# Optimization experiments

Hardware: AMD Instinct MI355X
Metric: run time of the kernel (lower is better)

The kernel has to match this reference:

```python
import jax, jax.numpy as jnp
import numpy as np

D_IN = 1024
D_OUT = 1024


def setup_inputs() -> dict:
    key = jax.random.key(0)
    kx, kq, kk, kv = jax.random.split(key, 4)
    x = jax.random.normal(kx, (4, 2048, D_IN), dtype=jnp.float32)
    s = 1.0 / np.sqrt(D_IN)
    Wq = jax.random.normal(kq, (D_IN, D_OUT), dtype=jnp.float32) * s
    Wk = jax.random.normal(kk, (D_IN, D_OUT), dtype=jnp.float32) * s
    Wv = jax.random.normal(kv, (D_IN, D_OUT), dtype=jnp.float32) * s
    return {"x": x, "Wq": Wq, "Wk": Wk, "Wv": Wv}


def reference(x, Wq, Wk, Wv):
    # x: [B, S, d_in]; W*: [d_in, d_out]
    B, S, _ = x.shape
    q = x @ Wq  # [B, S, d_out]
    k = x @ Wk
    v = x @ Wv
    scale = 1.0 / jnp.sqrt(jnp.asarray(k.shape[-1], x.dtype))
    scores = jnp.einsum("bqd,bkd->bqk", q, k) * scale  # [B, S, S]
    # causal mask: positions j > i masked to -inf (triu, diagonal=1)
    causal = jnp.tril(jnp.ones((S, S), dtype=bool))
    scores = jnp.where(causal[None, :, :], scores, -jnp.inf)
    attn = jax.nn.softmax(scores, axis=-1)  # dropout p=0.0 -> identity
    return jnp.einsum("bqk,bkd->bqd", attn, v)
```

## Files before the change

### kernel.cpp

```cpp
#include <hip/hip_runtime.h>
#include <hip/hip_bf16.h>

#define NB 4
#define SB 2048
#define DD 1024
#define BM 128
#define BN 128
#define BK 32

typedef __attribute__((ext_vector_type(8))) short bf16x8;
typedef __attribute__((ext_vector_type(4))) short bf16x4;
typedef __attribute__((ext_vector_type(4))) float f32x4;
typedef unsigned int u32;

__device__ __forceinline__ float bf2f(unsigned short u) {
    return __uint_as_float(((u32)u) << 16);
}
__device__ __forceinline__ short f2bf(float f) {
    u32 u = __float_as_uint(f);
    u32 r = (u + 0x7fffu + ((u >> 16) & 1u)) >> 16;
    return (short)r;
}

__device__ __forceinline__ void mfma_step(const short* As, const short* Bs,
                                          f32x4 (&acc)[4][4], int lane, int wave)
{
    const int wm = (wave >> 1) * 64, wn = (wave & 1) * 64;
    const int fr = lane & 15;
    const int quad = lane >> 4;
    bf16x8 af[4], bf[4];
#pragma unroll
    for (int t = 0; t < 4; t++) {
        af[t] = *(const bf16x8*)&As[(wm + t * 16 + fr) * BK + quad * 8];
        bf[t] = *(const bf16x8*)&Bs[(wn + t * 16 + fr) * BK + quad * 8];
    }
#pragma unroll
    for (int mt = 0; mt < 4; mt++)
#pragma unroll
        for (int nt = 0; nt < 4; nt++)
            acc[mt][nt] = __builtin_amdgcn_mfma_f32_16x16x32_bf16(
                af[mt], bf[nt], acc[mt][nt], 0, 0, 0);
}

__device__ __forceinline__ void mfma_step_pv(const short* As, const short* Bs,
                                             f32x4 (&acc)[2][4], int lane,
                                             int wave)
{
    const int wm = wave * 32;
    const int fr = lane & 15;
    const int quad = lane >> 4;
    bf16x8 af[2], bf[4];
#pragma unroll
    for (int t = 0; t < 2; t++)
        af[t] = *(const bf16x8*)&As[(wm + t * 16 + fr) * BK + quad * 8];
#pragma unroll
    for (int t = 0; t < 4; t++)
        bf[t] = *(const bf16x8*)&Bs[(t * 16 + fr) * BK + quad * 8];
#pragma unroll
    for (int mt = 0; mt < 2; mt++)
#pragma unroll
        for (int nt = 0; nt < 4; nt++)
            acc[mt][nt] = __builtin_amdgcn_mfma_f32_16x16x32_bf16(
                af[mt], bf[nt], acc[mt][nt], 0, 0, 0);
}

__device__ __forceinline__ void stage128x32(const short* __restrict__ g, int ld,
                                            short* lds, int tid) {
    const int wave = tid >> 6, lane = tid & 63;
    const int r = lane >> 2;
    const int c = (lane & 3) * 8;
#pragma unroll
    for (int i = 0; i < 2; i++) {
        const int chunk = wave * 2 + i;
        const short* gp = g + (size_t)(chunk * 16 + r) * ld + c;
        __builtin_amdgcn_global_load_lds(
            (const __attribute__((address_space(1))) u32*)gp,
            (__attribute__((address_space(3))) u32*)(lds + chunk * 512 + lane * 8),
            16, 0, 0);
    }
}

__device__ __forceinline__ void stage64x32(const short* __restrict__ g, int ld,
                                           short* lds, int tid) {
    const int wave = tid >> 6, lane = tid & 63;
    const int r = lane >> 2;
    const int c = (lane & 3) * 8;
    const short* gp = g + (size_t)(wave * 16 + r) * ld + c;
    __builtin_amdgcn_global_load_lds(
        (const __attribute__((address_space(1))) u32*)gp,
        (__attribute__((address_space(3))) u32*)(lds + wave * 512 + lane * 8),
        16, 0, 0);
}

__device__ __forceinline__ void stage_f32_128x32(const float* __restrict__ g,
                                                 int ld, short* lds, int tid) {
    const int r = tid >> 1;
    const int c = (tid & 1) * 16;
    const float* gp = &g[(size_t)r * ld + c];
    float4 v0 = *(const float4*)(gp + 0);
    float4 v1 = *(const float4*)(gp + 4);
    float4 v2 = *(const float4*)(gp + 8);
    float4 v3 = *(const float4*)(gp + 12);
    bf16x8 o0, o1;
    o0[0] = f2bf(v0.x); o0[1] = f2bf(v0.y); o0[2] = f2bf(v0.z); o0[3] = f2bf(v0.w);
    o0[4] = f2bf(v1.x); o0[5] = f2bf(v1.y); o0[6] = f2bf(v1.z); o0[7] = f2bf(v1.w);
    o1[0] = f2bf(v2.x); o1[1] = f2bf(v2.y); o1[2] = f2bf(v2.z); o1[3] = f2bf(v2.w);
    o1[4] = f2bf(v3.x); o1[5] = f2bf(v3.y); o1[6] = f2bf(v3.z); o1[7] = f2bf(v3.w);
    *(bf16x8*)&lds[r * BK + c] = o0;
    *(bf16x8*)&lds[r * BK + c + 8] = o1;
}

__device__ __forceinline__ void gemm_bt_body2(
    const short* __restrict__ A, int lda, const short* __restrict__ Bt, int ldb,
    int m0, int n0, int kend, short* As, short* Bs, f32x4 (&acc)[4][4], int tid)
{
    const int lane = tid & 63;
    const int wave = tid >> 6;
    const short* Ap = A + (size_t)m0 * lda;
    const short* Bp = Bt + (size_t)n0 * ldb;
    for (int k0 = 0; k0 < kend; k0 += 2 * BK) {
        stage128x32(Ap + k0, lda, As, tid);
        stage128x32(Ap + k0 + BK, lda, As + BM * BK, tid);
        stage128x32(Bp + k0, ldb, Bs, tid);
        stage128x32(Bp + k0 + BK, ldb, Bs + BN * BK, tid);
        __syncthreads();
        mfma_step(As, Bs, acc, lane, wave);
        mfma_step(As + BM * BK, Bs + BN * BK, acc, lane, wave);
        __syncthreads();
    }
}

__global__ __launch_bounds__(256) void prep_mm(
    const float* __restrict__ x, const float* __restrict__ Wq,
    const float* __restrict__ Wk, const float* __restrict__ Wv,
    short* __restrict__ xb, short* __restrict__ Wvt, float* __restrict__ Mp4)
{
    __shared__ short As[BM * BK], Bs[BN * BK];
    __shared__ short t[64][65];
    const int bx = blockIdx.x;
    const int tid = threadIdx.x;
    if (bx < 256) {
        const int ch = bx >> 6;
        const int t64 = bx & 63;
        const int m0 = (t64 >> 3) * BM;
        const int n0 = (t64 & 7) * BN;
        const int kbase = ch * 256;
        const int lane = tid & 63, wave = tid >> 6;
        f32x4 acc[4][4];
#pragma unroll
        for (int a = 0; a < 4; a++)
#pragma unroll
            for (int b = 0; b < 4; b++) acc[a][b] = (f32x4){0.f, 0.f, 0.f, 0.f};
        for (int k0 = 0; k0 < 256; k0 += BK) {
            stage_f32_128x32(Wk + (size_t)m0 * DD + kbase + k0, DD, As, tid);
            stage_f32_128x32(Wq + (size_t)n0 * DD + kbase + k0, DD, Bs, tid);
            __syncthreads();
            mfma_step(As, Bs, acc, lane, wave);
            __syncthreads();
        }
        const int wm = (wave >> 1) * 64, wn = (wave & 1) * 64;
        const int fr = lane & 15, quad = lane >> 4;
        float* Mc = Mp4 + (size_t)ch * DD * DD;
#pragma unroll
        for (int mt = 0; mt < 4; mt++)
#pragma unroll
            for (int nt = 0; nt < 4; nt++)
#pragma unroll
                for (int r = 0; r < 4; r++) {
                    const size_t m = m0 + wm + mt * 16 + quad * 4 + r;
                    const size_t n = n0 + wn + nt * 16 + fr;
                    Mc[m * DD + n] = acc[mt][nt][r];
                }
        return;
    }
    if (bx < 4352) {
        const size_t i = ((size_t)(bx - 256) * 256 + tid) * 8;
        float4 a = *(const float4*)&x[i];
        float4 b = *(const float4*)&x[i + 4];
        bf16x8 o;
        o[0] = f2bf(a.x); o[1] = f2bf(a.y); o[2] = f2bf(a.z); o[3] = f2bf(a.w);
        o[4] = f2bf(b.x); o[5] = f2bf(b.y); o[6] = f2bf(b.z); o[7] = f2bf(b.w);
        *(bf16x8*)&xb[i] = o;
        return;
    }
    const int rr = bx - 4352;
    const int k0 = (rr & 15) * 64;
    const int n0 = (rr >> 4) * 64;
    {
        const int r = tid >> 4;
        const int c = (tid & 15) * 4;
#pragma unroll
        for (int i = 0; i < 4; i++) {
            float4 v = *(const float4*)&Wv[(size_t)(k0 + i * 16 + r) * DD + n0 + c];
            t[i * 16 + r][c + 0] = f2bf(v.x);
            t[i * 16 + r][c + 1] = f2bf(v.y);
            t[i * 16 + r][c + 2] = f2bf(v.z);
            t[i * 16 + r][c + 3] = f2bf(v.w);
        }
    }
    __syncthreads();
    {
        const int r = tid >> 3;
        const int c = (tid & 7) * 8;
#pragma unroll
        for (int i = 0; i < 2; i++) {
            bf16x8 o;
#pragma unroll
            for (int j = 0; j < 8; j++) o[j] = t[c + j][i * 32 + r];
            *(bf16x8*)&Wvt[(size_t)(n0 + i * 32 + r) * DD + k0 + c] = o;
        }
    }
}

__global__ __launch_bounds__(256) void mm_reduce(const float* __restrict__ Mp4,
                                                 short* __restrict__ Mp)
{
    const size_t e = ((size_t)blockIdx.x * 256 + threadIdx.x) * 4;
    const size_t N = (size_t)DD * DD;
    float4 s = *(const float4*)&Mp4[e];
#pragma unroll
    for (int c = 1; c < 4; c++) {
        float4 p = *(const float4*)&Mp4[c * N + e];
        s.x += p.x; s.y += p.y; s.z += p.z; s.w += p.w;
    }
    bf16x4 o;
    o[0] = f2bf(s.x); o[1] = f2bf(s.y); o[2] = f2bf(s.z); o[3] = f2bf(s.w);
    *(bf16x4*)&Mp[e] = o;
}

__global__ __launch_bounds__(256) void tv_gemm(
    const short* __restrict__ xb, const short* __restrict__ Mp,
    const short* __restrict__ Wvt, short* __restrict__ T,
    short* __restrict__ Vt)
{
    __shared__ short As[2 * BM * BK], Bs[2 * BN * BK];
    const int lin = blockIdx.x + 8 * blockIdx.y;
    const int swz = (lin & 7) * 64 + (lin >> 3);
    const int n0 = (swz & 7) * BN;
    const int m0 = (swz >> 3) * BM;
    const int isv = blockIdx.z;
    const short* Bt = isv ? Wvt : Mp;
    f32x4 acc[4][4];
#pragma unroll
    for (int a = 0; a < 4; a++)
#pragma unroll
        for (int b = 0; b < 4; b++) acc[a][b] = (f32x4){0.f, 0.f, 0.f, 0.f};
    gemm_bt_body2(xb, DD, Bt, DD, m0, n0, DD, As, Bs, acc, threadIdx.x);
    const int lane = threadIdx.x & 63, wave = threadIdx.x >> 6;
    const int wm = (wave >> 1) * 64, wn = (wave & 1) * 64;
    const int fr = lane & 15, quad = lane >> 4;
    if (!isv) {
#pragma unroll
        for (int mt = 0; mt < 4; mt++)
#pragma unroll
            for (int nt = 0; nt < 4; nt++)
#pragma unroll
                for (int r = 0; r < 4; r++) {
                    const size_t m = m0 + wm + mt * 16 + quad * 4 + r;
                    const size_t n = n0 + wn + nt * 16 + fr;
                    T[m * DD + n] = f2bf(acc[mt][nt][r]);
                }
    } else {
        const int bb = m0 >> 11;
        const int s0 = (m0 & (SB - 1)) + wm + quad * 4;
        short* Vb = Vt + (size_t)bb * DD * SB;
#pragma unroll
        for (int mt = 0; mt < 4; mt++)
#pragma unroll
            for (int nt = 0; nt < 4; nt++) {
                const size_t n = n0 + wn + nt * 16 + fr;
                const size_t s = s0 + mt * 16;
                bf16x4 o;
#pragma unroll
                for (int r = 0; r < 4; r++) o[r] = f2bf(acc[mt][nt][r]);
                *(bf16x4*)&Vb[n * SB + s] = o;
            }
    }
}

__global__ __launch_bounds__(256) void scores_mfma(
    const short* __restrict__ T, const short* __restrict__ xb,
    short* __restrict__ Sc)
{
    const int bx = blockIdx.x;
    const int idx = (bx & 7) * 17 + (bx >> 3);
    int qt = (int)((__fsqrt_rn(8.f * idx + 1.f) - 1.f) * 0.5f);
    while ((qt + 1) * (qt + 2) / 2 <= idx) qt++;
    while (qt * (qt + 1) / 2 > idx) qt--;
    const int kt = idx - qt * (qt + 1) / 2;
    const int qm0 = qt * BM;
    const int kn0 = kt * BN;
    const int b = blockIdx.y;
    __shared__ short As[2 * BM * BK], Bs[2 * BN * BK];
    const short* Tb = T + (size_t)b * SB * DD;
    const short* Xb = xb + (size_t)b * SB * DD;
    short* Sb = Sc + (size_t)b * SB * SB;
    f32x4 acc[4][4];
#pragma unroll
    for (int a = 0; a < 4; a++)
#pragma unroll
        for (int c = 0; c < 4; c++) acc[a][c] = (f32x4){0.f, 0.f, 0.f, 0.f};
    gemm_bt_body2(Tb, DD, Xb, DD, qm0, kn0, DD, As, Bs, acc, threadIdx.x);
    const int lane = threadIdx.x & 63, wave = threadIdx.x >> 6;
    const int wm = (wave >> 1) * 64, wn = (wave & 1) * 64;
    const int fr = lane & 15, quad = lane >> 4;
    const float scale = 0.03125f;
#pragma unroll
    for (int mt = 0; mt < 4; mt++)
#pragma unroll
        for (int nt = 0; nt < 4; nt++)
#pragma unroll
            for (int r = 0; r < 4; r++) {
                const size_t q = qm0 + wm + mt * 16 + quad * 4 + r;
                const size_t k = kn0 + wn + nt * 16 + fr;
                Sb[q * SB + k] = f2bf(acc[mt][nt][r] * scale);
            }
}

__global__ __launch_bounds__(256) void softmax_kernel(short* __restrict__ Sc)
{
    const int row = blockIdx.x;
    const int i = row & (SB - 1);
    const int jlim = ((i >> 7) + 1) << 7;
    short* r = Sc + (size_t)row * SB;
    const int t = threadIdx.x;
    const int lane = t & 63, wave = t >> 6;
    __shared__ float red[8];

    const int j0 = t * 8;
    bf16x8 in = {0, 0, 0, 0, 0, 0, 0, 0};
    if (j0 <= i) in = *(const bf16x8*)&r[j0];
    float v[8];
    float mx = -1e30f;
#pragma unroll
    for (int e = 0; e < 8; e++) {
        const float s = (j0 + e <= i) ? bf2f((unsigned short)in[e]) : -1e30f;
        v[e] = s;
        mx = fmaxf(mx, s);
    }
#pragma unroll
    for (int o = 32; o > 0; o >>= 1) mx = fmaxf(mx, __shfl_down(mx, o));
    if (lane == 0) red[wave] = mx;
    __syncthreads();
    mx = fmaxf(fmaxf(red[0], red[1]), fmaxf(red[2], red[3]));

    float sum = 0.f;
#pragma unroll
    for (int e = 0; e < 8; e++) {
        const float x = (j0 + e <= i) ? __expf(v[e] - mx) : 0.f;
        v[e] = x;
        sum += x;
    }
#pragma unroll
    for (int o = 32; o > 0; o >>= 1) sum += __shfl_down(sum, o);
    if (lane == 0) red[4 + wave] = sum;
    __syncthreads();
    const float inv = 1.0f / (red[4] + red[5] + red[6] + red[7]);
    if (j0 < jlim) {
        bf16x8 o;
#pragma unroll
        for (int e = 0; e < 8; e++) o[e] = f2bf(v[e] * inv);
        *(bf16x8*)&r[j0] = o;
    }
}

__global__ __launch_bounds__(256) void pv_mfma(
    const short* __restrict__ P, const short* __restrict__ Vt,
    float* __restrict__ O)
{
    __shared__ short As[2 * BM * BK], Bs[2 * 64 * BK];
    const int n0 = blockIdx.x * 64;
    const int pair = blockIdx.y;
    const int b = blockIdx.z;
    const short* Pb = P + (size_t)b * SB * SB;
    const short* Vb = Vt + (size_t)b * DD * SB;
    float* Ob = O + (size_t)b * SB * DD;
    const int tid = threadIdx.x;
    const int lane = tid & 63, wave = tid >> 6;
    const int fr = lane & 15, quad = lane >> 4;
    for (int half = 0; half < 2; ++half) {
        const int qt = half ? (15 - pair) : pair;
        const int qm0 = qt * BM;
        const int kend = (qt + 1) * BM;
        const short* Pq = Pb + (size_t)qm0 * SB;
        const short* Vn = Vb + (size_t)n0 * SB;
        f32x4 acc[2][4];
#pragma unroll
        for (int a = 0; a < 2; a++)
#pragma unroll
            for (int c = 0; c < 4; c++) acc[a][c] = (f32x4){0.f, 0.f, 0.f, 0.f};
        for (int k0 = 0; k0 < kend; k0 += 2 * BK) {
            stage128x32(Pq + k0, SB, As, tid);
            stage128x32(Pq + k0 + BK, SB, As + BM * BK, tid);
            stage64x32(Vn + k0, SB, Bs, tid);
            stage64x32(Vn + k0 + BK, SB, Bs + 64 * BK, tid);
            __syncthreads();
            mfma_step_pv(As, Bs, acc, lane, wave);
            mfma_step_pv(As + BM * BK, Bs + 64 * BK, acc, lane, wave);
            __syncthreads();
        }
#pragma unroll
        for (int mt = 0; mt < 2; mt++)
#pragma unroll
            for (int nt = 0; nt < 4; nt++)
#pragma unroll
                for (int r = 0; r < 4; r++) {
                    const size_t q = qm0 + wave * 32 + mt * 16 + quad * 4 + r;
                    const size_t n = n0 + nt * 16 + fr;
                    Ob[q * DD + n] = acc[mt][nt][r];
                }
    }
}

extern "C" void kernel_launch(void* const* d_in, const int* in_sizes, int n_in,
                              void* d_out, int out_size, void* d_ws, size_t ws_size,
                              hipStream_t stream)
{
    const float* x  = (const float*)d_in[0];
    const float* Wq = (const float*)d_in[1];
    const float* Wk = (const float*)d_in[2];
    const float* Wv = (const float*)d_in[3];
    float* out = (float*)d_out;

    const size_t XE = (size_t)NB * SB * DD;
    const size_t WE = (size_t)DD * DD;
    short* xb  = (short*)d_ws;
    short* T   = xb + XE;
    short* Vt  = T + XE;
    short* Sc  = Vt + XE;
    float* Pp  = (float*)(Sc + (size_t)NB * SB * SB);
    short* Wvt = (short*)(Pp + (size_t)NB * 1024 * DD);
    short* Mp  = Wvt + WE;
    float* Mp4 = (float*)Sc;

    prep_mm<<<dim3(256 + 4096 + 256), 256, 0, stream>>>(
        x, Wq, Wk, Wv, xb, Wvt, Mp4);
    mm_reduce<<<dim3(1024), 256, 0, stream>>>(Mp4, Mp);
    tv_gemm<<<dim3(DD / BN, (NB * SB) / BM, 2), 256, 0, stream>>>(
        xb, Mp, Wvt, T, Vt);
    scores_mfma<<<dim3(136, NB), 256, 0, stream>>>(T, xb, Sc);
    softmax_kernel<<<dim3(NB * SB), 256, 0, stream>>>(Sc);
    pv_mfma<<<dim3(DD / 64, 8, NB), 256, 0, stream>>>(Sc, Vt, out);
}
```

Measured before the change: 231.2 us.

## Double-buffer LDS staging with manual vmcnt waits in GEMM and PV loops

Replaces the load-all-then-compute loops, which handled two K-slices per iteration, with a software-pipelined double-buffered loop. It prefetches the next BK slice into the alternate LDS buffer while MFMAs run on the current one. Explicit s_waitcnt vmcnt counts and raw s_barrier calls replace __syncthreads, so only the older loads must finish before the barrier. The aim is to hide global-load latency behind matrix math. The risk is that the hand-set vmcnt values assume a fixed number of outstanding loads per stage, and any extra compiler-emitted memory operation would break that.

```diff
diff --git a/kernel.cpp b/kernel.cpp
--- a/kernel.cpp
+++ b/kernel.cpp
@@ -20,6 +20,20 @@
     u32 u = __float_as_uint(f);
     u32 r = (u + 0x7fffu + ((u >> 16) & 1u)) >> 16;
     return (short)r;
+}
+
+__device__ __forceinline__ void wait_vm4() {
+    asm volatile("s_waitcnt vmcnt(4)" ::: "memory");
+}
+__device__ __forceinline__ void wait_vm3() {
+    asm volatile("s_waitcnt vmcnt(3)" ::: "memory");
+}
+__device__ __forceinline__ void wait_vm0() {
+    asm volatile("s_waitcnt vmcnt(0)" ::: "memory");
+}
+__device__ __forceinline__ void barrier_raw() {
+    __builtin_amdgcn_s_barrier();
+    asm volatile("" ::: "memory");
 }
 
 __device__ __forceinline__ void mfma_step(const short* As, const short* Bs,
@@ -110,23 +124,28 @@
     *(bf16x8*)&lds[r * BK + c + 8] = o1;
 }
 
-__device__ __forceinline__ void gemm_bt_body2(
+__device__ __forceinline__ void gemm_bt_cnt(
     const short* __restrict__ A, int lda, const short* __restrict__ Bt, int ldb,
-    int m0, int n0, int kend, short* As, short* Bs, f32x4 (&acc)[4][4], int tid)
+    int kend, short* As, short* Bs, f32x4 (&acc)[4][4], int tid)
 {
     const int lane = tid & 63;
     const int wave = tid >> 6;
-    const short* Ap = A + (size_t)m0 * lda;
-    const short* Bp = Bt + (size_t)n0 * ldb;
-    for (int k0 = 0; k0 < kend; k0 += 2 * BK) {
-        stage128x32(Ap + k0, lda, As, tid);
-        stage128x32(Ap + k0 + BK, lda, As + BM * BK, tid);
-        stage128x32(Bp + k0, ldb, Bs, tid);
-        stage128x32(Bp + k0 + BK, ldb, Bs + BN * BK, tid);
-        __syncthreads();
-        mfma_step(As, Bs, acc, lane, wave);
-        mfma_step(As + BM * BK, Bs + BN * BK, acc, lane, wave);
-        __syncthreads();
+    stage128x32(A, lda, As, tid);
+    stage128x32(Bt, ldb, Bs, tid);
+    for (int k0 = 0; k0 < kend; k0 += BK) {
+        const int cur = (k0 >> 5) & 1;
+        const short* as = As + cur * (BM * BK);
+        const short* bs = Bs + cur * (BN * BK);
+        if (k0 + BK < kend) {
+            stage128x32(A + k0 + BK, lda, As + (cur ^ 1) * (BM * BK), tid);
+            stage128x32(Bt + k0 + BK, ldb, Bs + (cur ^ 1) * (BN * BK), tid);
+            wait_vm4();
+        } else {
+            wait_vm0();
+        }
+        barrier_raw();
+        mfma_step(as, bs, acc, lane, wave);
+        barrier_raw();
     }
 }
 
@@ -245,7 +264,8 @@
     for (int a = 0; a < 4; a++)
 #pragma unroll
         for (int b = 0; b < 4; b++) acc[a][b] = (f32x4){0.f, 0.f, 0.f, 0.f};
-    gemm_bt_body2(xb, DD, Bt, DD, m0, n0, DD, As, Bs, acc, threadIdx.x);
+    gemm_bt_cnt(xb + (size_t)m0 * DD, DD, Bt + (size_t)n0 * DD, DD, DD,
+                As, Bs, acc, threadIdx.x);
     const int lane = threadIdx.x & 63, wave = threadIdx.x >> 6;
     const int wm = (wave >> 1) * 64, wn = (wave & 1) * 64;
     const int fr = lane & 15, quad = lane >> 4;
@@ -300,7 +320,8 @@
     for (int a = 0; a < 4; a++)
 #pragma unroll
         for (int c = 0; c < 4; c++) acc[a][c] = (f32x4){0.f, 0.f, 0.f, 0.f};
-    gemm_bt_body2(Tb, DD, Xb, DD, qm0, kn0, DD, As, Bs, acc, threadIdx.x);
+    gemm_bt_cnt(Tb + (size_t)qm0 * DD, DD, Xb + (size_t)kn0 * DD, DD, DD,
+                As, Bs, acc, threadIdx.x);
     const int lane = threadIdx.x & 63, wave = threadIdx.x >> 6;
     const int wm = (wave >> 1) * 64, wn = (wave & 1) * 64;
     const int fr = lane & 15, quad = lane >> 4;
@@ -389,15 +410,22 @@
         for (int a = 0; a < 2; a++)
 #pragma unroll
             for (int c = 0; c < 4; c++) acc[a][c] = (f32x4){0.f, 0.f, 0.f, 0.f};
-        for (int k0 = 0; k0 < kend; k0 += 2 * BK) {
-            stage128x32(Pq + k0, SB, As, tid);
-            stage128x32(Pq + k0 + BK, SB, As + BM * BK, tid);
-            stage64x32(Vn + k0, SB, Bs, tid);
-            stage64x32(Vn + k0 + BK, SB, Bs + 64 * BK, tid);
-            __syncthreads();
-            mfma_step_pv(As, Bs, acc, lane, wave);
-            mfma_step_pv(As + BM * BK, Bs + 64 * BK, acc, lane, wave);
-            __syncthreads();
+        stage128x32(Pq, SB, As, tid);
+        stage64x32(Vn, SB, Bs, tid);
+        for (int k0 = 0; k0 < kend; k0 += BK) {
+            const int cur = (k0 >> 5) & 1;
+            const short* as = As + cur * (BM * BK);
+            const short* bs = Bs + cur * (64 * BK);
+            if (k0 + BK < kend) {
+                stage128x32(Pq + k0 + BK, SB, As + (cur ^ 1) * (BM * BK), tid);
+                stage64x32(Vn + k0 + BK, SB, Bs + (cur ^ 1) * (64 * BK), tid);
+                wait_vm3();
+            } else {
+                wait_vm0();
+            }
+            barrier_raw();
+            mfma_step_pv(as, bs, acc, lane, wave);
+            barrier_raw();
         }
 #pragma unroll
         for (int mt = 0; mt < 2; mt++)
```

New measurement: 245.9 us. +6.3%, slower.

## Double-buffer PV global-to-LDS loads and retile scores kernel to 128x64 blocks

Applied to the files above, without the earlier changes.

The PV kernel now keeps two LDS buffers and prefetches the next K chunk while computing the current one. It uses raw barriers with explicit vmcnt waits, so global loads overlap MFMA work. The scores kernel switches from 128x128 to 128x64 causal tiles, doubling the grid to 272 blocks per batch for better occupancy and load balance. This assumes the stage helpers issue direct global-to-LDS loads that vmcnt(6) correctly tracks. It also doubles LDS use in pv_mfma, which may reduce occupancy.

```diff
diff --git a/kernel.cpp b/kernel.cpp
--- a/kernel.cpp
+++ b/kernel.cpp
@@ -20,6 +20,17 @@
     u32 u = __float_as_uint(f);
     u32 r = (u + 0x7fffu + ((u >> 16) & 1u)) >> 16;
     return (short)r;
+}
+
+__device__ __forceinline__ void wait_vm6() {
+    asm volatile("s_waitcnt vmcnt(6)" ::: "memory");
+}
+__device__ __forceinline__ void wait_vm0() {
+    asm volatile("s_waitcnt vmcnt(0)" ::: "memory");
+}
+__device__ __forceinline__ void barrier_raw() {
+    __builtin_amdgcn_s_barrier();
+    asm volatile("" ::: "memory");
 }
 
 __device__ __forceinline__ void mfma_step(const short* As, const short* Bs,
@@ -283,36 +294,45 @@
     short* __restrict__ Sc)
 {
     const int bx = blockIdx.x;
-    const int idx = (bx & 7) * 17 + (bx >> 3);
-    int qt = (int)((__fsqrt_rn(8.f * idx + 1.f) - 1.f) * 0.5f);
-    while ((qt + 1) * (qt + 2) / 2 <= idx) qt++;
-    while (qt * (qt + 1) / 2 > idx) qt--;
-    const int kt = idx - qt * (qt + 1) / 2;
+    const int idx = (bx & 7) * 34 + (bx >> 3);
+    int qt = (int)((__fsqrt_rn(4.f * idx + 1.f) - 1.f) * 0.5f);
+    while ((qt + 1) * (qt + 2) <= idx) qt++;
+    while (qt * (qt + 1) > idx) qt--;
+    const int kt = idx - qt * (qt + 1);
     const int qm0 = qt * BM;
-    const int kn0 = kt * BN;
+    const int kn0 = kt * 64;
     const int b = blockIdx.y;
-    __shared__ short As[2 * BM * BK], Bs[2 * BN * BK];
-    const short* Tb = T + (size_t)b * SB * DD;
-    const short* Xb = xb + (size_t)b * SB * DD;
+    __shared__ short As[2 * BM * BK], Bs[2 * 64 * BK];
+    const short* Tq = T + (size_t)b * SB * DD + (size_t)qm0 * DD;
+    const short* Xk = xb + (size_t)b * SB * DD + (size_t)kn0 * DD;
     short* Sb = Sc + (size_t)b * SB * SB;
-    f32x4 acc[4][4];
-#pragma unroll
-    for (int a = 0; a < 4; a++)
+    const int tid = threadIdx.x;
+    const int lane = tid & 63, wave = tid >> 6;
+    f32x4 acc[2][4];
+#pragma unroll
+    for (int a = 0; a < 2; a++)
 #pragma unroll
         for (int c = 0; c < 4; c++) acc[a][c] = (f32x4){0.f, 0.f, 0.f, 0.f};
-    gemm_bt_body2(Tb, DD, Xb, DD, qm0, kn0, DD, As, Bs, acc, threadIdx.x);
-    const int lane = threadIdx.x & 63, wave = threadIdx.x >> 6;
-    const int wm = (wave >> 1) * 64, wn = (wave & 1) * 64;
+    for (int k0 = 0; k0 < DD; k0 += 2 * BK) {
+        stage128x32(Tq + k0, DD, As, tid);
+        stage128x32(Tq + k0 + BK, DD, As + BM * BK, tid);
+        stage64x32(Xk + k0, DD, Bs, tid);
+        stage64x32(Xk + k0 + BK, DD, Bs + 64 * BK, tid);
+        __syncthreads();
+        mfma_step_pv(As, Bs, acc, lane, wave);
+        mfma_step_pv(As + BM * BK, Bs + 64 * BK, acc, lane, wave);
+        __syncthreads();
+    }
     const int fr = lane & 15, quad = lane >> 4;
     const float scale = 0.03125f;
 #pragma unroll
-    for (int mt = 0; mt < 4; mt++)
+    for (int mt = 0; mt < 2; mt++)
 #pragma unroll
         for (int nt = 0; nt < 4; nt++)
 #pragma unroll
             for (int r = 0; r < 4; r++) {
-                const size_t q = qm0 + wm + mt * 16 + quad * 4 + r;
-                const size_t k = kn0 + wn + nt * 16 + fr;
+                const size_t q = qm0 + wave * 32 + mt * 16 + quad * 4 + r;
+                const size_t k = kn0 + nt * 16 + fr;
                 Sb[q * SB + k] = f2bf(acc[mt][nt][r] * scale);
             }
 }
@@ -368,7 +388,8 @@
     const short* __restrict__ P, const short* __restrict__ Vt,
     float* __restrict__ O)
 {
-    __shared__ short As[2 * BM * BK], Bs[2 * 64 * BK];
+    __shared__ short As[4 * BM * BK];
+    __shared__ short Bs[4 * 64 * BK];
     const int n0 = blockIdx.x * 64;
     const int pair = blockIdx.y;
     const int b = blockIdx.z;
@@ -381,7 +402,7 @@
     for (int half = 0; half < 2; ++half) {
         const int qt = half ? (15 - pair) : pair;
         const int qm0 = qt * BM;
-        const int kend = (qt + 1) * BM;
+        const int nj = (qt + 1) * 2;
         const short* Pq = Pb + (size_t)qm0 * SB;
         const short* Vn = Vb + (size_t)n0 * SB;
         f32x4 acc[2][4];
@@ -389,15 +410,30 @@
         for (int a = 0; a < 2; a++)
 #pragma unroll
             for (int c = 0; c < 4; c++) acc[a][c] = (f32x4){0.f, 0.f, 0.f, 0.f};
-        for (int k0 = 0; k0 < kend; k0 += 2 * BK) {
-            stage128x32(Pq + k0, SB, As, tid);
-            stage128x32(Pq + k0 + BK, SB, As + BM * BK, tid);
-            stage64x32(Vn + k0, SB, Bs, tid);
-            stage64x32(Vn + k0 + BK, SB, Bs + 64 * BK, tid);
-            __syncthreads();
-            mfma_step_pv(As, Bs, acc, lane, wave);
-            mfma_step_pv(As + BM * BK, Bs + 64 * BK, acc, lane, wave);
-            __syncthreads();
+        stage128x32(Pq, SB, As, tid);
+        stage128x32(Pq + BK, SB, As + BM * BK, tid);
+        stage64x32(Vn, SB, Bs, tid);
+        stage64x32(Vn + BK, SB, Bs + 64 * BK, tid);
+        for (int j = 0; j < nj; ++j) {
+            const int cur = j & 1;
+            const short* as = As + cur * (2 * BM * BK);
+            const short* bs = Bs + cur * (2 * 64 * BK);
+            if (j + 1 < nj) {
+                const int off = (j + 1) * 64;
+                short* an = As + (cur ^ 1) * (2 * BM * BK);
+                short* bn = Bs + (cur ^ 1) * (2 * 64 * BK);
+                stage128x32(Pq + off, SB, an, tid);
+                stage128x32(Pq + off + BK, SB, an + BM * BK, tid);
+                stage64x32(Vn + off, SB, bn, tid);
+                stage64x32(Vn + off + BK, SB, bn + 64 * BK, tid);
+                wait_vm6();
+            } else {
+                wait_vm0();
+            }
+            barrier_raw();
+            mfma_step_pv(as, bs, acc, lane, wave);
+            mfma_step_pv(as + BM * BK, bs + 64 * BK, acc, lane, wave);
+            barrier_raw();
         }
 #pragma unroll
         for (int mt = 0; mt < 2; mt++)
@@ -438,7 +474,7 @@
     mm_reduce<<<dim3(1024), 256, 0, stream>>>(Mp4, Mp);
     tv_gemm<<<dim3(DD / BN, (NB * SB) / BM, 2), 256, 0, stream>>>(
         xb, Mp, Wvt, T, Vt);
-    scores_mfma<<<dim3(136, NB), 256, 0, stream>>>(T, xb, Sc);
+    scores_mfma<<<dim3(272, NB), 256, 0, stream>>>(T, xb, Sc);
     softmax_kernel<<<dim3(NB * SB), 256, 0, stream>>>(Sc);
     pv_mfma<<<dim3(DD / 64, 8, NB), 256, 0, stream>>>(Sc, Vt, out);
 }
```

New measurement: 231.0 us. About the same (-0.1%).
